# Kernel optimization log

Measured on AMD Instinct MI355X. Metric: run time of the kernel, lower is better.

## Reference

```python
import jax, jax.numpy as jnp
import numpy as np

B, N, C, E, H = 2, 20000, 64, 640000, 16

def setup_inputs() -> dict:
    key = jax.random.key(0)
    ks = jax.random.split(key, 9)
    Q = jax.random.normal(ks[0], (B, N, C), dtype=jnp.float32)
    K = jax.random.normal(ks[1], (B, N, C), dtype=jnp.float32)
    V = jax.random.normal(ks[2], (B, N, C), dtype=jnp.float32)
    src = jax.random.randint(ks[3], (E,), 0, N, dtype=jnp.int32)
    dst = jax.random.randint(ks[4], (E,), 0, N, dtype=jnp.int32)
    efeat = jax.random.uniform(ks[5], (E, 2), dtype=jnp.float32)  # [s_norm, d_norm] in [0,1]
    W1 = jax.random.normal(ks[6], (2, H), dtype=jnp.float32) * 0.5
    b1 = jnp.zeros((H,), dtype=jnp.float32)
    W2 = jax.random.normal(ks[7], (H, 1), dtype=jnp.float32) * 0.5
    b2 = jnp.zeros((1,), dtype=jnp.float32)
    return {"Q": Q, "K": K, "V": V, "efeat": efeat, "W1": W1, "b1": b1,
            "W2": W2, "b2": b2, "src": src, "dst": dst}

def reference(Q, K, V, efeat, W1, b1, W2, b2, src, dst):
    n = Q.shape[1]
    # per-edge bias: MLP(e_ij) -> (E,)
    bias = (jax.nn.relu(efeat @ W1 + b1) @ W2 + b2)[:, 0]
    # per-edge logits: Q_dst . K_src  -> (E, B)
    logits = jnp.einsum('bec,bec->eb', Q[:, dst, :], K[:, src, :]) + bias[:, None]
    # segment softmax over incoming edges of each dst node
    seg_max = jax.ops.segment_max(logits, dst, num_segments=n)          # (N, B)
    exp_l = jnp.exp(logits - seg_max[dst])                               # (E, B)
    denom = jax.ops.segment_sum(exp_l, dst, num_segments=n)[dst]         # (E, B)
    alpha = exp_l / denom                                                # (E, B)
    # weighted aggregation of parent values: (E,B,C) scattered to (N,B,C)
    msg = alpha[:, :, None] * jnp.transpose(V[:, src, :], (1, 0, 2))
    H_msg = jax.ops.segment_sum(msg, dst, num_segments=n)                # (N, B, C)
    return jnp.transpose(H_msg, (1, 0, 2))                               # (B, N, C)
```

## Files before the change

### kernel.cpp

```cpp
#include <hip/hip_runtime.h>
#include <hip/hip_fp16.h>
#include <math.h>


#define EB_B 2
#define EB_C 64
#define EB_H 16

__device__ __forceinline__ unsigned f2h2(float a, float b) {
    __half2 h = __floats2half2_rn(a, b);
    return *reinterpret_cast<unsigned*>(&h);
}
__device__ __forceinline__ float2 h2f2(unsigned u) {
    __half2 h = *reinterpret_cast<__half2*>(&u);
    return __half22float2(h);
}

__global__ __launch_bounds__(256) void eb_pack_kernel(
    const float4* __restrict__ K4, const float4* __restrict__ V4,
    uint4* __restrict__ kv, int total, int* __restrict__ cnt, int N) {
    int i = blockIdx.x * blockDim.x + threadIdx.x;
    if (i < N) cnt[i] = 0;
    if (i >= total) return;
    float4 k = K4[i];
    float4 v = V4[i];
    uint4 o;
    o.x = f2h2(k.x, k.y);
    o.y = f2h2(k.z, k.w);
    o.z = f2h2(v.x, v.y);
    o.w = f2h2(v.z, v.w);
    kv[i] = o;
}

__global__ void eb_count_kernel(const int* __restrict__ dst,
                                int* __restrict__ cnt,
                                int* __restrict__ slot, int E) {
    int e = blockIdx.x * blockDim.x + threadIdx.x;
    if (e < E) slot[e] = atomicAdd(&cnt[dst[e]], 1);
}

__global__ __launch_bounds__(1024) void eb_scan1(const int* __restrict__ cnt,
                                                 int* __restrict__ offsets,
                                                 int* __restrict__ bsum, int N) {
    __shared__ int wsum[16];
    int tid = threadIdx.x;
    int wv = tid >> 6, ln = tid & 63;
    int i = blockIdx.x * 1024 + tid;
    int v = (i < N) ? cnt[i] : 0;
    int x = v;
#pragma unroll
    for (int off = 1; off < 64; off <<= 1) {
        int t = __shfl_up(x, off, 64);
        if (ln >= off) x += t;
    }
    if (ln == 63) wsum[wv] = x;
    __syncthreads();
    if (wv == 0 && ln < 16) {
        int y = wsum[ln];
#pragma unroll
        for (int off = 1; off < 16; off <<= 1) {
            int t = __shfl_up(y, off, 64);
            if (ln >= off) y += t;
        }
        wsum[ln] = y;
    }
    __syncthreads();
    int base = (wv > 0 ? wsum[wv - 1] : 0);
    if (i < N) offsets[i] = base + x - v;
    if (tid == 1023) bsum[blockIdx.x] = base + x;
}

__global__ __launch_bounds__(1024) void eb_scan3(int* __restrict__ offsets,
                                                 const int* __restrict__ bsum,
                                                 int N, int E) {
    __shared__ int s_base;
    if (threadIdx.x == 0) {
        int b = 0;
        for (int j = 0; j < (int)blockIdx.x; ++j) b += bsum[j];
        s_base = b;
    }
    __syncthreads();
    int i = blockIdx.x * 1024 + threadIdx.x;
    if (i < N) offsets[i] += s_base;
    else if (i == N) offsets[N] = E;
}

__global__ void eb_fill_kernel(const int* __restrict__ dst,
                               const int* __restrict__ src,
                               const int* __restrict__ slot,
                               const int* __restrict__ offsets,
                               const float* __restrict__ efeat,
                               const float* __restrict__ W1,
                               const float* __restrict__ b1,
                               const float* __restrict__ W2,
                               const float* __restrict__ b2,
                               int2* __restrict__ ep, int E) {
    int e = blockIdx.x * blockDim.x + threadIdx.x;
    if (e >= E) return;
    float ef0 = efeat[2 * e];
    float ef1 = efeat[2 * e + 1];
    float acc = b2[0];
#pragma unroll
    for (int h = 0; h < EB_H; ++h) {
        float a = fmaf(ef0, W1[h], fmaf(ef1, W1[EB_H + h], b1[h]));
        a = fmaxf(a, 0.0f);
        acc = fmaf(a, W2[h], acc);
    }
    int pos = offsets[dst[e]] + slot[e];
    ep[pos] = make_int2(src[e], __float_as_int(acc));
}

__global__ __launch_bounds__(256) void eb_attn_fp16_kernel(
    const float4* __restrict__ Q4, const uint4* __restrict__ kv,
    const int2* __restrict__ ep, const int* __restrict__ offsets,
    float4* __restrict__ out4, int N) {
    int wave = threadIdx.x >> 6;
    int lane = threadIdx.x & 63;
    int task = blockIdx.x * 4 + wave;
    if (task >= N * EB_B) return;
    int b = (task >= N) ? 1 : 0;
    int n = task - (b ? N : 0);
    int g = lane >> 4;
    int cl = lane & 15;
    const size_t brow = (size_t)N * 16;
    float4 q = Q4[(size_t)b * brow + (size_t)n * 16 + cl];
    const uint4* kvb = kv + (size_t)b * brow;
    int start = offsets[n];
    int end = offsets[n + 1];
    int nit = (end - start + 7) >> 3;

    float m = -1e30f, s = 0.0f;
    float ax = 0.0f, ay = 0.0f, az = 0.0f, aw = 0.0f;

    for (int it = 0; it < nit; ++it) {
        int e0 = start + it * 8 + g;
        int e1 = e0 + 4;
        bool v0 = e0 < end;
        bool v1 = e1 < end;
        int2 md0 = ep[v0 ? e0 : 0];
        int2 md1 = ep[v1 ? e1 : 0];
        uint4 u0 = kvb[(size_t)md0.x * 16 + cl];
        uint4 u1 = kvb[(size_t)md1.x * 16 + cl];
        float2 k0a = h2f2(u0.x), k0b = h2f2(u0.y);
        float2 k1a = h2f2(u1.x), k1b = h2f2(u1.y);
        float p0 = fmaf(q.x, k0a.x, fmaf(q.y, k0a.y,
                   fmaf(q.z, k0b.x, q.w * k0b.y)));
        float p1 = fmaf(q.x, k1a.x, fmaf(q.y, k1a.y,
                   fmaf(q.z, k1b.x, q.w * k1b.y)));
        p0 += __shfl_xor(p0, 1);  p1 += __shfl_xor(p1, 1);
        p0 += __shfl_xor(p0, 2);  p1 += __shfl_xor(p1, 2);
        p0 += __shfl_xor(p0, 4);  p1 += __shfl_xor(p1, 4);
        p0 += __shfl_xor(p0, 8);  p1 += __shfl_xor(p1, 8);
        float l0 = v0 ? p0 + __int_as_float(md0.y) : -INFINITY;
        float l1 = v1 ? p1 + __int_as_float(md1.y) : -INFINITY;
        float mn = fmaxf(m, fmaxf(l0, l1));
        float sc = __expf(m - mn);
        float w0 = __expf(l0 - mn);
        float w1 = __expf(l1 - mn);
        float2 va0 = h2f2(u0.z), vb0 = h2f2(u0.w);
        float2 va1 = h2f2(u1.z), vb1 = h2f2(u1.w);
        s  = fmaf(s, sc, w0 + w1);
        ax = fmaf(ax, sc, fmaf(w0, va0.x, w1 * va1.x));
        ay = fmaf(ay, sc, fmaf(w0, va0.y, w1 * va1.y));
        az = fmaf(az, sc, fmaf(w0, vb0.x, w1 * vb1.x));
        aw = fmaf(aw, sc, fmaf(w0, vb0.y, w1 * vb1.y));
        m = mn;
    }

    float m1 = fmaxf(m, __shfl_xor(m, 16));
    float mA = fmaxf(m1, __shfl_xor(m1, 32));
    float scale = __expf(m - mA);
    s *= scale; ax *= scale; ay *= scale; az *= scale; aw *= scale;
    s  += __shfl_xor(s, 16);  s  += __shfl_xor(s, 32);
    ax += __shfl_xor(ax, 16); ax += __shfl_xor(ax, 32);
    ay += __shfl_xor(ay, 16); ay += __shfl_xor(ay, 32);
    az += __shfl_xor(az, 16); az += __shfl_xor(az, 32);
    aw += __shfl_xor(aw, 16); aw += __shfl_xor(aw, 32);

    if (lane < 16) {
        float inv = (end > start) ? 1.0f / s : 0.0f;
        float4 o;
        o.x = ax * inv; o.y = ay * inv; o.z = az * inv; o.w = aw * inv;
        out4[(size_t)b * brow + (size_t)n * 16 + cl] = o;
    }
}

__global__ __launch_bounds__(256) void eb_attn_f32_kernel(
    const float4* __restrict__ Q4, const float4* __restrict__ K4,
    const float4* __restrict__ V4,
    const int2* __restrict__ ep, const int* __restrict__ offsets,
    float4* __restrict__ out4, int N) {
    int wave = threadIdx.x >> 6;
    int lane = threadIdx.x & 63;
    int task = blockIdx.x * 4 + wave;
    if (task >= N * EB_B) return;
    int b = (task >= N) ? 1 : 0;
    int n = task - (b ? N : 0);
    int g = lane >> 4;
    int cl = lane & 15;
    const size_t brow = (size_t)N * 16;
    const float4* Qb = Q4 + (size_t)b * brow;
    const float4* Kb = K4 + (size_t)b * brow;
    const float4* Vb = V4 + (size_t)b * brow;
    float4 q = Qb[(size_t)n * 16 + cl];
    int start = offsets[n];
    int end = offsets[n + 1];
    int nit = (end - start + 3) >> 2;

    float m = -1e30f, s = 0.0f;
    float ax = 0.0f, ay = 0.0f, az = 0.0f, aw = 0.0f;
    for (int it = 0; it < nit; ++it) {
        int ei = start + it * 4 + g;
        bool valid = ei < end;
        int2 md = ep[valid ? ei : 0];
        int sv = md.x;
        float4 k = Kb[(size_t)sv * 16 + cl];
        float4 v = Vb[(size_t)sv * 16 + cl];
        float p = fmaf(q.x, k.x, fmaf(q.y, k.y, fmaf(q.z, k.z, q.w * k.w)));
        p += __shfl_xor(p, 1);
        p += __shfl_xor(p, 2);
        p += __shfl_xor(p, 4);
        p += __shfl_xor(p, 8);
        float l = valid ? p + __int_as_float(md.y) : -INFINITY;
        float mn = fmaxf(m, l);
        float sc = __expf(m - mn);
        float w  = __expf(l - mn);
        s  = fmaf(s, sc, w);
        ax = fmaf(ax, sc, w * v.x);
        ay = fmaf(ay, sc, w * v.y);
        az = fmaf(az, sc, w * v.z);
        aw = fmaf(aw, sc, w * v.w);
        m = mn;
    }
    float m1 = fmaxf(m, __shfl_xor(m, 16));
    float mA = fmaxf(m1, __shfl_xor(m1, 32));
    float scale = __expf(m - mA);
    s *= scale; ax *= scale; ay *= scale; az *= scale; aw *= scale;
    s  += __shfl_xor(s, 16);  s  += __shfl_xor(s, 32);
    ax += __shfl_xor(ax, 16); ax += __shfl_xor(ax, 32);
    ay += __shfl_xor(ay, 16); ay += __shfl_xor(ay, 32);
    az += __shfl_xor(az, 16); az += __shfl_xor(az, 32);
    aw += __shfl_xor(aw, 16); aw += __shfl_xor(aw, 32);
    if (lane < 16) {
        float inv = (end > start) ? 1.0f / s : 0.0f;
        float4 o;
        o.x = ax * inv; o.y = ay * inv; o.z = az * inv; o.w = aw * inv;
        out4[(size_t)b * brow + (size_t)n * 16 + cl] = o;
    }
}

extern "C" void kernel_launch(void* const* d_in, const int* in_sizes, int n_in,
                              void* d_out, int out_size, void* d_ws, size_t ws_size,
                              hipStream_t stream) {
    const float* Q     = (const float*)d_in[0];
    const float* K     = (const float*)d_in[1];
    const float* V     = (const float*)d_in[2];
    const float* efeat = (const float*)d_in[3];
    const float* W1    = (const float*)d_in[4];
    const float* b1    = (const float*)d_in[5];
    const float* W2    = (const float*)d_in[6];
    const float* b2    = (const float*)d_in[7];
    const int*   src   = (const int*)d_in[8];
    const int*   dst   = (const int*)d_in[9];
    float* out = (float*)d_out;

    const int E = in_sizes[8];
    const int N = in_sizes[0] / (EB_B * EB_C);

    char* base = (char*)d_ws;
    size_t off = 0;
    auto take = [&](size_t nbytes) {
        char* p = base + off;
        off += (nbytes + 15) & ~(size_t)15;
        return p;
    };
    int* offsets = (int*)take((size_t)(N + 1) * 4);
    int* cnt     = (int*)take((size_t)N * 4);
    int* bsum    = (int*)take(64 * 4);
    int* slot    = (int*)take((size_t)E * 4);
    int2* ep     = (int2*)take((size_t)E * 8);
    uint4* kv    = (uint4*)take((size_t)EB_B * N * 16 * sizeof(uint4));
    bool use_fp16 = off <= ws_size;

    int tpb = 256;
    int NB = (N + 1023) >> 10;
    if (use_fp16) {
        int total = EB_B * N * 16;
        eb_pack_kernel<<<(total + tpb - 1) / tpb, tpb, 0, stream>>>(
            (const float4*)K, (const float4*)V, kv, total, cnt, N);
    } else {
        eb_pack_kernel<<<(N + tpb - 1) / tpb, tpb, 0, stream>>>(
            (const float4*)K, (const float4*)V, kv, 0, cnt, N);
    }
    eb_count_kernel<<<(E + tpb - 1) / tpb, tpb, 0, stream>>>(dst, cnt, slot, E);
    eb_scan1<<<NB, 1024, 0, stream>>>(cnt, offsets, bsum, N);
    eb_scan3<<<(N + 1024) >> 10, 1024, 0, stream>>>(offsets, bsum, N, E);
    eb_fill_kernel<<<(E + tpb - 1) / tpb, tpb, 0, stream>>>(
        dst, src, slot, offsets, efeat, W1, b1, W2, b2, ep, E);

    int tasks = N * EB_B;
    if (use_fp16) {
        eb_attn_fp16_kernel<<<(tasks + 3) / 4, tpb, 0, stream>>>(
            (const float4*)Q, kv, ep, offsets, (float4*)out, N);
    } else {
        eb_attn_f32_kernel<<<(tasks + 3) / 4, tpb, 0, stream>>>(
            (const float4*)Q, (const float4*)K, (const float4*)V,
            ep, offsets, (float4*)out, N);
    }
}
```

Baseline: 99.09 us.

## Split fused attention into separate K-logit and V-aggregation passes

```diff
diff --git a/kernel.cpp b/kernel.cpp
--- a/kernel.cpp
+++ b/kernel.cpp
@@ -16,20 +16,26 @@
     return __half22float2(h);
 }
 
-__global__ __launch_bounds__(256) void eb_pack_kernel(
+__global__ __launch_bounds__(256) void eb_pack(
     const float4* __restrict__ K4, const float4* __restrict__ V4,
-    uint4* __restrict__ kv, int total, int* __restrict__ cnt, int N) {
+    uint2* __restrict__ kpk, uint2* __restrict__ vpk,
+    uint4* __restrict__ kv, int total,
+    int* __restrict__ cnt, int* __restrict__ flags, int N, int mode) {
     int i = blockIdx.x * blockDim.x + threadIdx.x;
     if (i < N) cnt[i] = 0;
+    if (i < 32) flags[i] = 0;
     if (i >= total) return;
     float4 k = K4[i];
     float4 v = V4[i];
-    uint4 o;
-    o.x = f2h2(k.x, k.y);
-    o.y = f2h2(k.z, k.w);
-    o.z = f2h2(v.x, v.y);
-    o.w = f2h2(v.z, v.w);
-    kv[i] = o;
+    if (mode) {
+        kpk[i] = make_uint2(f2h2(k.x, k.y), f2h2(k.z, k.w));
+        vpk[i] = make_uint2(f2h2(v.x, v.y), f2h2(v.z, v.w));
+    } else {
+        uint4 o;
+        o.x = f2h2(k.x, k.y); o.y = f2h2(k.z, k.w);
+        o.z = f2h2(v.x, v.y); o.w = f2h2(v.z, v.w);
+        kv[i] = o;
+    }
 }
 
 __global__ void eb_count_kernel(const int* __restrict__ dst,
@@ -39,19 +45,21 @@
     if (e < E) slot[e] = atomicAdd(&cnt[dst[e]], 1);
 }
 
-__global__ __launch_bounds__(1024) void eb_scan1(const int* __restrict__ cnt,
-                                                 int* __restrict__ offsets,
-                                                 int* __restrict__ bsum, int N) {
+__global__ __launch_bounds__(1024) void eb_scan(const int* __restrict__ cnt,
+                                                int* __restrict__ offsets,
+                                                int* __restrict__ flags,
+                                                int N, int E) {
     __shared__ int wsum[16];
-    int tid = threadIdx.x;
-    int wv = tid >> 6, ln = tid & 63;
-    int i = blockIdx.x * 1024 + tid;
+    __shared__ int s_agg, s_base;
+    const int b = blockIdx.x, t = threadIdx.x;
+    const int ln = t & 63, wv = t >> 6;
+    const int i = (b << 10) + t;
     int v = (i < N) ? cnt[i] : 0;
     int x = v;
 #pragma unroll
     for (int off = 1; off < 64; off <<= 1) {
-        int t = __shfl_up(x, off, 64);
-        if (ln >= off) x += t;
+        int tv = __shfl_up(x, off, 64);
+        if (ln >= off) x += tv;
     }
     if (ln == 63) wsum[wv] = x;
     __syncthreads();
@@ -59,29 +67,26 @@
         int y = wsum[ln];
 #pragma unroll
         for (int off = 1; off < 16; off <<= 1) {
-            int t = __shfl_up(y, off, 64);
-            if (ln >= off) y += t;
+            int tv = __shfl_up(y, off, 64);
+            if (ln >= off) y += tv;
         }
         wsum[ln] = y;
     }
     __syncthreads();
-    int base = (wv > 0 ? wsum[wv - 1] : 0);
-    if (i < N) offsets[i] = base + x - v;
-    if (tid == 1023) bsum[blockIdx.x] = base + x;
-}
-
-__global__ __launch_bounds__(1024) void eb_scan3(int* __restrict__ offsets,
-                                                 const int* __restrict__ bsum,
-                                                 int N, int E) {
-    __shared__ int s_base;
-    if (threadIdx.x == 0) {
-        int b = 0;
-        for (int j = 0; j < (int)blockIdx.x; ++j) b += bsum[j];
-        s_base = b;
-    }
+    if (t == 1023) s_agg = wsum[15];
     __syncthreads();
-    int i = blockIdx.x * 1024 + threadIdx.x;
-    if (i < N) offsets[i] += s_base;
+    if (t == 0) {
+        int base = 0;
+        if (b > 0) {
+            while ((base = atomicAdd(&flags[b - 1], 0)) == 0) {}
+            base -= 1;
+        }
+        atomicExch(&flags[b], base + s_agg + 1);
+        s_base = base;
+    }
+    __syncthreads();
+    int local_excl = (wv > 0 ? wsum[wv - 1] : 0) + x - v;
+    if (i < N) offsets[i] = s_base + local_excl;
     else if (i == N) offsets[N] = E;
 }
 
@@ -89,7 +94,7 @@
                                const int* __restrict__ src,
                                const int* __restrict__ slot,
                                const int* __restrict__ offsets,
-                               const float* __restrict__ efeat,
+                               const float2* __restrict__ efeat2,
                                const float* __restrict__ W1,
                                const float* __restrict__ b1,
                                const float* __restrict__ W2,
@@ -97,17 +102,125 @@
                                int2* __restrict__ ep, int E) {
     int e = blockIdx.x * blockDim.x + threadIdx.x;
     if (e >= E) return;
-    float ef0 = efeat[2 * e];
-    float ef1 = efeat[2 * e + 1];
+    float2 ef = efeat2[e];
     float acc = b2[0];
 #pragma unroll
     for (int h = 0; h < EB_H; ++h) {
-        float a = fmaf(ef0, W1[h], fmaf(ef1, W1[EB_H + h], b1[h]));
+        float a = fmaf(ef.x, W1[h], fmaf(ef.y, W1[EB_H + h], b1[h]));
         a = fmaxf(a, 0.0f);
         acc = fmaf(a, W2[h], acc);
     }
     int pos = offsets[dst[e]] + slot[e];
     ep[pos] = make_int2(src[e], __float_as_int(acc));
+}
+
+__global__ __launch_bounds__(256) void eb_attn_k(
+    const float4* __restrict__ Q4, const uint2* __restrict__ kpk,
+    const int2* __restrict__ ep, const int* __restrict__ offsets,
+    float* __restrict__ logits, float2* __restrict__ ms, int N, int E) {
+    int wave = threadIdx.x >> 6;
+    int lane = threadIdx.x & 63;
+    int task = blockIdx.x * 4 + wave;
+    if (task >= N * EB_B) return;
+    int b = (task >= N) ? 1 : 0;
+    int n = task - (b ? N : 0);
+    int g = lane >> 4;
+    int cl = lane & 15;
+    float4 q = Q4[((size_t)b * N + n) * 16 + cl];
+    const uint2* kb = kpk + (size_t)b * N * 16;
+    float* lgb = logits + (size_t)b * E;
+    int start = offsets[n];
+    int end = offsets[n + 1];
+    int nit = (end - start + 7) >> 3;
+
+    float m = -1e30f, s = 0.0f;
+    for (int it = 0; it < nit; ++it) {
+        int e0 = start + it * 8 + g;
+        int e1 = e0 + 4;
+        bool v0 = e0 < end;
+        bool v1 = e1 < end;
+        int2 md0 = ep[v0 ? e0 : 0];
+        int2 md1 = ep[v1 ? e1 : 0];
+        uint2 u0 = kb[(size_t)md0.x * 16 + cl];
+        uint2 u1 = kb[(size_t)md1.x * 16 + cl];
+        float2 a0 = h2f2(u0.x), b0 = h2f2(u0.y);
+        float2 a1 = h2f2(u1.x), b1_ = h2f2(u1.y);
+        float p0 = fmaf(q.x, a0.x, fmaf(q.y, a0.y, fmaf(q.z, b0.x, q.w * b0.y)));
+        float p1 = fmaf(q.x, a1.x, fmaf(q.y, a1.y, fmaf(q.z, b1_.x, q.w * b1_.y)));
+        p0 += __shfl_xor(p0, 1);  p1 += __shfl_xor(p1, 1);
+        p0 += __shfl_xor(p0, 2);  p1 += __shfl_xor(p1, 2);
+        p0 += __shfl_xor(p0, 4);  p1 += __shfl_xor(p1, 4);
+        p0 += __shfl_xor(p0, 8);  p1 += __shfl_xor(p1, 8);
+        float l0 = v0 ? p0 + __int_as_float(md0.y) : -INFINITY;
+        float l1 = v1 ? p1 + __int_as_float(md1.y) : -INFINITY;
+        if (cl == 0) {
+            if (v0) lgb[e0] = l0;
+            if (v1) lgb[e1] = l1;
+        }
+        float mn = fmaxf(m, fmaxf(l0, l1));
+        float sc = __expf(m - mn);
+        s = fmaf(s, sc, __expf(l0 - mn) + __expf(l1 - mn));
+        m = mn;
+    }
+    float m1 = fmaxf(m, __shfl_xor(m, 16));
+    float mA = fmaxf(m1, __shfl_xor(m1, 32));
+    s *= __expf(m - mA);
+    s += __shfl_xor(s, 16);
+    s += __shfl_xor(s, 32);
+    if (lane == 0) ms[(size_t)b * N + n] = make_float2(mA, s);
+}
+
+__global__ __launch_bounds__(256) void eb_attn_v(
+    const uint2* __restrict__ vpk, const int2* __restrict__ ep,
+    const int* __restrict__ offsets, const float* __restrict__ logits,
+    const float2* __restrict__ ms, float4* __restrict__ out4, int N, int E) {
+    int wave = threadIdx.x >> 6;
+    int lane = threadIdx.x & 63;
+    int task = blockIdx.x * 4 + wave;
+    if (task >= N * EB_B) return;
+    int b = (task >= N) ? 1 : 0;
+    int n = task - (b ? N : 0);
+    int g = lane >> 4;
+    int cl = lane & 15;
+    const uint2* vb = vpk + (size_t)b * N * 16;
+    const float* lgb = logits + (size_t)b * E;
+    int start = offsets[n];
+    int end = offsets[n + 1];
+    int nit = (end - start + 7) >> 3;
+    float2 msv = ms[(size_t)b * N + n];
+    float m = msv.x;
+
+    float ax = 0.0f, ay = 0.0f, az = 0.0f, aw = 0.0f;
+    for (int it = 0; it < nit; ++it) {
+        int e0 = start + it * 8 + g;
+        int e1 = e0 + 4;
+        bool v0 = e0 < end;
+        bool v1 = e1 < end;
+        int2 md0 = ep[v0 ? e0 : 0];
+        int2 md1 = ep[v1 ? e1 : 0];
+        float l0 = lgb[v0 ? e0 : 0];
+        float l1 = lgb[v1 ? e1 : 0];
+        uint2 u0 = vb[(size_t)md0.x * 16 + cl];
+        uint2 u1 = vb[(size_t)md1.x * 16 + cl];
+        float w0 = v0 ? __expf(l0 - m) : 0.0f;
+        float w1 = v1 ? __expf(l1 - m) : 0.0f;
+        float2 a0 = h2f2(u0.x), b0 = h2f2(u0.y);
+        float2 a1 = h2f2(u1.x), b1_ = h2f2(u1.y);
+        ax = fmaf(w0, a0.x, fmaf(w1, a1.x, ax));
+        ay = fmaf(w0, a0.y, fmaf(w1, a1.y, ay));
+        az = fmaf(w0, b0.x, fmaf(w1, b1_.x, az));
+        aw = fmaf(w0, b0.y, fmaf(w1, b1_.y, aw));
+    }
+    ax += __shfl_xor(ax, 16); ax += __shfl_xor(ax, 32);
+    ay += __shfl_xor(ay, 16); ay += __shfl_xor(ay, 32);
+    az += __shfl_xor(az, 16); az += __shfl_xor(az, 32);
+    aw += __shfl_xor(aw, 16); aw += __shfl_xor(aw, 32);
+    if (lane < 16) {
+        float inv = (end > start) ? 1.0f / msv.y : 0.0f;
+        float4 o;
+        o.x = ax * inv; o.y = ay * inv; o.z = az * inv; o.w = aw * inv;
+        out4[((size_t)b * N + n) * 16 + cl] = o;
+    }
 }
 
 __global__ __launch_bounds__(256) void eb_attn_fp16_kernel(
@@ -131,7 +244,6 @@
 
     float m = -1e30f, s = 0.0f;
     float ax = 0.0f, ay = 0.0f, az = 0.0f, aw = 0.0f;
-
     for (int it = 0; it < nit; ++it) {
         int e0 = start + it * 8 + g;
         int e1 = e0 + 4;
@@ -166,72 +278,6 @@
         aw = fmaf(aw, sc, fmaf(w0, vb0.y, w1 * vb1.y));
         m = mn;
     }
-
-    float m1 = fmaxf(m, __shfl_xor(m, 16));
-    float mA = fmaxf(m1, __shfl_xor(m1, 32));
-    float scale = __expf(m - mA);
-    s *= scale; ax *= scale; ay *= scale; az *= scale; aw *= scale;
-    s  += __shfl_xor(s, 16);  s  += __shfl_xor(s, 32);
-    ax += __shfl_xor(ax, 16); ax += __shfl_xor(ax, 32);
-    ay += __shfl_xor(ay, 16); ay += __shfl_xor(ay, 32);
-    az += __shfl_xor(az, 16); az += __shfl_xor(az, 32);
-    aw += __shfl_xor(aw, 16); aw += __shfl_xor(aw, 32);
-
-    if (lane < 16) {
-        float inv = (end > start) ? 1.0f / s : 0.0f;
-        float4 o;
-        o.x = ax * inv; o.y = ay * inv; o.z = az * inv; o.w = aw * inv;
-        out4[(size_t)b * brow + (size_t)n * 16 + cl] = o;
-    }
-}
-
-__global__ __launch_bounds__(256) void eb_attn_f32_kernel(
-    const float4* __restrict__ Q4, const float4* __restrict__ K4,
-    const float4* __restrict__ V4,
-    const int2* __restrict__ ep, const int* __restrict__ offsets,
-    float4* __restrict__ out4, int N) {
-    int wave = threadIdx.x >> 6;
-    int lane = threadIdx.x & 63;
-    int task = blockIdx.x * 4 + wave;
-    if (task >= N * EB_B) return;
-    int b = (task >= N) ? 1 : 0;
-    int n = task - (b ? N : 0);
-    int g = lane >> 4;
-    int cl = lane & 15;
-    const size_t brow = (size_t)N * 16;
-    const float4* Qb = Q4 + (size_t)b * brow;
-    const float4* Kb = K4 + (size_t)b * brow;
-    const float4* Vb = V4 + (size_t)b * brow;
-    float4 q = Qb[(size_t)n * 16 + cl];
-    int start = offsets[n];
-    int end = offsets[n + 1];
-    int nit = (end - start + 3) >> 2;
-
-    float m = -1e30f, s = 0.0f;
-    float ax = 0.0f, ay = 0.0f, az = 0.0f, aw = 0.0f;
-    for (int it = 0; it < nit; ++it) {
-        int ei = start + it * 4 + g;
-        bool valid = ei < end;
-        int2 md = ep[valid ? ei : 0];
-        int sv = md.x;
-        float4 k = Kb[(size_t)sv * 16 + cl];
-        float4 v = Vb[(size_t)sv * 16 + cl];
-        float p = fmaf(q.x, k.x, fmaf(q.y, k.y, fmaf(q.z, k.z, q.w * k.w)));
-        p += __shfl_xor(p, 1);
-        p += __shfl_xor(p, 2);
-        p += __shfl_xor(p, 4);
-        p += __shfl_xor(p, 8);
-        float l = valid ? p + __int_as_float(md.y) : -INFINITY;
-        float mn = fmaxf(m, l);
-        float sc = __expf(m - mn);
-        float w  = __expf(l - mn);
-        s  = fmaf(s, sc, w);
-        ax = fmaf(ax, sc, w * v.x);
-        ay = fmaf(ay, sc, w * v.y);
-        az = fmaf(az, sc, w * v.z);
-        aw = fmaf(aw, sc, w * v.w);
-        m = mn;
-    }
     float m1 = fmaxf(m, __shfl_xor(m, 16));
     float mA = fmaxf(m1, __shfl_xor(m1, 32));
     float scale = __expf(m - mA);
@@ -252,20 +298,21 @@
 extern "C" void kernel_launch(void* const* d_in, const int* in_sizes, int n_in,
                               void* d_out, int out_size, void* d_ws, size_t ws_size,
                               hipStream_t stream) {
-    const float* Q     = (const float*)d_in[0];
-    const float* K     = (const float*)d_in[1];
-    const float* V     = (const float*)d_in[2];
-    const float* efeat = (const float*)d_in[3];
-    const float* W1    = (const float*)d_in[4];
-    const float* b1    = (const float*)d_in[5];
-    const float* W2    = (const float*)d_in[6];
-    const float* b2    = (const float*)d_in[7];
-    const int*   src   = (const int*)d_in[8];
-    const int*   dst   = (const int*)d_in[9];
-    float* out = (float*)d_out;
+    const float4* Q4  = (const float4*)d_in[0];
+    const float4* K4  = (const float4*)d_in[1];
+    const float4* V4  = (const float4*)d_in[2];
+    const float2* ef2 = (const float2*)d_in[3];
+    const float* W1   = (const float*)d_in[4];
+    const float* b1   = (const float*)d_in[5];
+    const float* W2   = (const float*)d_in[6];
+    const float* b2   = (const float*)d_in[7];
+    const int*   src  = (const int*)d_in[8];
+    const int*   dst  = (const int*)d_in[9];
+    float4* out4 = (float4*)d_out;
 
     const int E = in_sizes[8];
     const int N = in_sizes[0] / (EB_B * EB_C);
+    const int total = EB_B * N * 16;
 
     char* base = (char*)d_ws;
     size_t off = 0;
@@ -276,35 +323,37 @@
     };
     int* offsets = (int*)take((size_t)(N + 1) * 4);
     int* cnt     = (int*)take((size_t)N * 4);
-    int* bsum    = (int*)take(64 * 4);
+    int* flags   = (int*)take(32 * 4);
     int* slot    = (int*)take((size_t)E * 4);
     int2* ep     = (int2*)take((size_t)E * 8);
-    uint4* kv    = (uint4*)take((size_t)EB_B * N * 16 * sizeof(uint4));
-    bool use_fp16 = off <= ws_size;
+    size_t prefix = off;
+    float* logits = (float*)take((size_t)EB_B * E * 4);
+    float2* ms    = (float2*)take((size_t)EB_B * N * 8);
+    uint2* kpk    = (uint2*)take((size_t)total * 8);
+    uint2* vpk    = (uint2*)take((size_t)total * 8);
+    size_t split_bytes = off;
+    off = prefix;
+    uint4* kv = (uint4*)take((size_t)total * 16);
+    size_t kv_bytes = off;
+
+    int mode = (split_bytes <= ws_size) ? 1 : 0;
+    (void)kv_bytes;
 
     int tpb = 256;
     int NB = (N + 1023) >> 10;
-    if (use_fp16) {
-        int total = EB_B * N * 16;
-        eb_pack_kernel<<<(total + tpb - 1) / tpb, tpb, 0, stream>>>(
-            (const float4*)K, (const float4*)V, kv, total, cnt, N);
+    eb_pack<<<(total + tpb - 1) / tpb, tpb, 0, stream>>>(
+        K4, V4, kpk, vpk, kv, total, cnt, flags, N, mode);
+    eb_count_kernel<<<(E + tpb - 1) / tpb, tpb, 0, stream>>>(dst, cnt, slot, E);
+    eb_scan<<<NB, 1024, 0, stream>>>(cnt, offsets, flags, N, E);
+    eb_fill_kernel<<<(E + tpb - 1) / tpb, tpb, 0, stream>>>(
+        dst, src, slot, offsets, ef2, W1, b1, W2, b2, ep, E);
+
+    int tasks = N * EB_B;
+    int blks = (tasks + 3) / 4;
+    if (mode) {
+        eb_attn_k<<<blks, tpb, 0, stream>>>(Q4, kpk, ep, offsets, logits, ms, N, E);
+        eb_attn_v<<<blks, tpb, 0, stream>>>(vpk, ep, offsets, logits, ms, out4, N, E);
     } else {
-        eb_pack_kernel<<<(N + tpb - 1) / tpb, tpb, 0, stream>>>(
-            (const float4*)K, (const float4*)V, kv, 0, cnt, N);
-    }
-    eb_count_kernel<<<(E + tpb - 1) / tpb, tpb, 0, stream>>>(dst, cnt, slot, E);
-    eb_scan1<<<NB, 1024, 0, stream>>>(cnt, offsets, bsum, N);
-    eb_scan3<<<(N + 1024) >> 10, 1024, 0, stream>>>(offsets, bsum, N, E);
-    eb_fill_kernel<<<(E + tpb - 1) / tpb, tpb, 0, stream>>>(
-        dst, src, slot, offsets, efeat, W1, b1, W2, b2, ep, E);
-
-    int tasks = N * EB_B;
-    if (use_fp16) {
-        eb_attn_fp16_kernel<<<(tasks + 3) / 4, tpb, 0, stream>>>(
-            (const float4*)Q, kv, ep, offsets, (float4*)out, N);
-    } else {
-        eb_attn_f32_kernel<<<(tasks + 3) / 4, tpb, 0, stream>>>(
-            (const float4*)Q, (const float4*)K, (const float4*)V,
-            ep, offsets, (float4*)out, N);
-    }
-}
+        eb_attn_fp16_kernel<<<blks, tpb, 0, stream>>>(Q4, kv, ep, offsets, out4, N);
+    }
+}
```

Measured after the change: 129.0 us. 1.3x slower.
